# Performance work log

Measured on AMD Instinct MI355X. Metric: run time of the kernel, lower is better.

The kernel has to match this reference:

```python
import jax, jax.numpy as jnp
import numpy as np

B, T = 32, 2048
HID, ACT, SRC, AGE = 512, 64, 2, 16
TRUNK, BINS, PHASES = 256, 20, 7
IN_DIM = HID + ACT + SRC + AGE  # 594


def setup_inputs() -> dict:
    key = jax.random.key(0)
    ks = jax.random.split(key, 16)
    s_in = 1.0 / np.sqrt(IN_DIM)
    s_tr = 1.0 / np.sqrt(TRUNK)
    s_h = 1.0 / np.sqrt(HID)
    return {
        "h_t": jax.random.normal(ks[0], (B, T, HID), jnp.float32),
        "a_t": jax.random.normal(ks[1], (B, T, ACT), jnp.float32),
        "d_t": jax.random.normal(ks[2], (B, T, SRC), jnp.float32),
        "age_embed": jax.random.normal(ks[3], (B, T, AGE), jnp.float32),
        "trunk_w": jax.random.normal(ks[4], (IN_DIM, TRUNK), jnp.float32) * s_in,
        "trunk_b": jax.random.normal(ks[5], (TRUNK,), jnp.float32) * s_in,
        "inst_base_w": jax.random.normal(ks[6], (TRUNK, BINS), jnp.float32) * s_tr,
        "inst_base_b": jax.random.normal(ks[7], (BINS,), jnp.float32) * s_tr,
        "group_base_w": jax.random.normal(ks[8], (TRUNK, BINS), jnp.float32) * s_tr,
        "group_base_b": jax.random.normal(ks[9], (BINS,), jnp.float32) * s_tr,
        "inst_exp_w": jax.random.normal(ks[10], (PHASES, TRUNK, BINS), jnp.float32) * s_tr,
        "inst_exp_b": jax.random.normal(ks[11], (PHASES, BINS), jnp.float32) * s_tr,
        "group_exp_w": jax.random.normal(ks[12], (PHASES, TRUNK, BINS), jnp.float32) * s_tr,
        "group_exp_b": jax.random.normal(ks[13], (PHASES, BINS), jnp.float32) * s_tr,
        "router_w": jax.random.normal(ks[14], (HID, PHASES), jnp.float32) * s_h,
        "router_b": jax.random.normal(ks[15], (PHASES,), jnp.float32) * s_h,
    }


def reference(h_t, a_t, d_t, age_embed,
              trunk_w, trunk_b, inst_base_w, inst_base_b,
              group_base_w, group_base_b, inst_exp_w, inst_exp_b,
              group_exp_w, group_exp_b, router_w, router_b):
    # Shared trunk: Linear(594,256) -> exact GELU
    x = jnp.concatenate([h_t, a_t, d_t, age_embed], axis=-1)  # [B,T,594]
    z = jax.nn.gelu(jnp.einsum('bti,io->bto', x, trunk_w) + trunk_b,
                    approximate=False)  # [B,T,256]

    # Soft phase routing from h_t
    pw = jax.nn.softmax(jnp.einsum('bth,hp->btp', h_t, router_w) + router_b,
                        axis=-1)  # [B,T,7]

    # Base heads
    inst_base = jnp.einsum('btd,dk->btk', z, inst_base_w) + inst_base_b
    group_base = jnp.einsum('btd,dk->btk', z, group_base_w) + group_base_b

    # All 7 experts as one batched GEMM, then weighted reduction over phases
    inst_e = jnp.einsum('btd,pdk->btpk', z, inst_exp_w) + inst_exp_b  # [B,T,7,20]
    group_e = jnp.einsum('btd,pdk->btpk', z, group_exp_w) + group_exp_b
    inst_res = jnp.einsum('btp,btpk->btk', pw, inst_e)
    group_res = jnp.einsum('btp,btpk->btk', pw, group_e)

    return (inst_base + inst_res, group_base + group_res)
```

## Files before the change

kernel.cpp:

```cpp
#include <hip/hip_runtime.h>
#include <math.h>

typedef unsigned int uint;
typedef unsigned short ushort;

using short8 = __attribute__((ext_vector_type(8))) short;
using f32x4  = __attribute__((ext_vector_type(4))) float;

#define BT      65536
#define HID     512
#define IN_DIM  594
#define TRUNK   256
#define BINS    20
#define NKCH    19
#define NCOMBO  320

#define WT_P_SZ (19*16*64*8)
#define RP_SZ   (16*64*8)
#define WA_P_SZ (8*20*64*8)

__device__ inline ushort f2bf(float f) {
    uint u = __float_as_uint(f);
    return (ushort)((u + 0x7fffu + ((u >> 16) & 1u)) >> 16);
}

__global__ __launch_bounds__(64) void pack_all(
    const float* __restrict__ trunk_w, const float* __restrict__ router_w,
    const float* __restrict__ inst_base_w, const float* __restrict__ inst_base_b,
    const float* __restrict__ group_base_w, const float* __restrict__ group_base_b,
    const float* __restrict__ inst_exp_w, const float* __restrict__ inst_exp_b,
    const float* __restrict__ group_exp_w, const float* __restrict__ group_exp_b,
    ushort* __restrict__ WtP, ushort* __restrict__ RP,
    ushort* __restrict__ WaP, float* __restrict__ wbias)
{
    const int b = blockIdx.x, l = threadIdx.x;
    const int lr = l & 15, lg = l >> 4;
    if (b < 304) {
        int kk = b >> 4, n = b & 15;
        int col = n * 16 + lr;
        ushort* dst = WtP + ((size_t)(kk * 16 + n) * 64 + l) * 8;
        #pragma unroll
        for (int j = 0; j < 8; ++j) {
            int k = kk * 32 + lg * 8 + j;
            dst[j] = (k < IN_DIM) ? f2bf(trunk_w[k * TRUNK + col]) : (ushort)0;
        }
    } else if (b < 320) {
        int kk = b - 304;
        ushort* dst = RP + ((size_t)(kk * 64 + l)) * 8;
        #pragma unroll
        for (int j = 0; j < 8; ++j) {
            int k = kk * 32 + lg * 8 + j;
            dst[j] = (lr < 7) ? f2bf(router_w[k * 7 + lr]) : (ushort)0;
        }
    } else if (b < 480) {
        int b2 = b - 320, kk = b2 / 20, n = b2 % 20;
        int combo = n * 16 + lr;
        int h = combo / 160, rem = combo % 160, kb = rem >> 3, p = rem & 7;
        const float* bw = h ? group_base_w : inst_base_w;
        const float* ew = h ? group_exp_w  : inst_exp_w;
        ushort* dst = WaP + ((size_t)(kk * 20 + n) * 64 + l) * 8;
        #pragma unroll
        for (int j = 0; j < 8; ++j) {
            int k = kk * 32 + lg * 8 + j;
            float v = (p == 0) ? bw[k * BINS + kb]
                               : ew[((p - 1) * TRUNK + k) * BINS + kb];
            dst[j] = f2bf(v);
        }
    } else {
        for (int c = l; c < NCOMBO; c += 64) {
            int h = c / 160, rem = c % 160, kb = rem >> 3, p = rem & 7;
            const float* bb = h ? group_base_b : inst_base_b;
            const float* eb = h ? group_exp_b  : inst_exp_b;
            wbias[c] = (p == 0) ? bb[kb] : eb[(p - 1) * BINS + kb];
        }
    }
}

__global__ __launch_bounds__(256, 2) void fused_mfma(
    const float* __restrict__ h_t, const float* __restrict__ a_t,
    const float* __restrict__ d_t, const float* __restrict__ age,
    const float* __restrict__ trunk_b, const float* __restrict__ router_b,
    const ushort* __restrict__ WtP, const ushort* __restrict__ RP,
    const ushort* __restrict__ WaP, const float* __restrict__ wbias,
    float* __restrict__ out)
{
    __shared__ alignas(16) ushort smem[32768];

    const int tid = threadIdx.x;
    const int l = tid & 63, w = tid >> 6;
    const int lr = l & 15, lg = l >> 4;
    const int block0 = blockIdx.x * 128;

    const int srow = tid >> 1;
    const int scb  = (tid & 1) * 16;
    const int stok = block0 + srow;

    f32x4 acc[2][16];
    f32x4 accr[2];
    #pragma unroll
    for (int m = 0; m < 2; ++m) {
        accr[m] = (f32x4){0.f, 0.f, 0.f, 0.f};
        #pragma unroll
        for (int n = 0; n < 16; ++n) acc[m][n] = (f32x4){0.f, 0.f, 0.f, 0.f};
    }

    auto stage_load = [&](int kk, float4 ld[4]) {
        int c0 = kk * 32 + scb;
        if (kk < 16) {
            const float4* p = (const float4*)(h_t + (size_t)stok * HID + c0);
            ld[0] = p[0]; ld[1] = p[1]; ld[2] = p[2]; ld[3] = p[3];
        } else if (kk < 18) {
            const float4* p = (const float4*)(a_t + (size_t)stok * 64 + (c0 - 512));
            ld[0] = p[0]; ld[1] = p[1]; ld[2] = p[2]; ld[3] = p[3];
        } else {
            float* f = (float*)ld;
            #pragma unroll
            for (int j = 0; j < 16; ++j) {
                int c = c0 + j;
                float v;
                if (c < 578)        v = d_t[(size_t)stok * 2 + (c - 576)];
                else if (c < 594)   v = age[(size_t)stok * 16 + (c - 578)];
                else                v = 0.f;
                f[j] = v;
            }
        }
    };
    auto stage_write = [&](int buf, float4 ld[4]) {
        const float* f = (const float*)ld;
        short8 v0, v1;
        #pragma unroll
        for (int j = 0; j < 8; ++j) {
            v0[j] = (short)f2bf(f[j]);
            v1[j] = (short)f2bf(f[j + 8]);
        }
        ushort* dst = smem + buf * 4096 + srow * 32 + scb;
        *(short8*)dst = v0;
        *(short8*)(dst + 8) = v1;
    };

    {
        float4 ld[4];
        stage_load(0, ld);
        stage_write(0, ld);
        __syncthreads();
        int cur = 0;
        for (int kk = 0; kk < NKCH; ++kk) {
            float4 nld[4];
            if (kk < NKCH - 1) stage_load(kk + 1, nld);

            const ushort* xa = smem + cur * 4096;
            short8 a0 = *(const short8*)(xa + (w * 32 + lr) * 32 + lg * 8);
            short8 a1 = *(const short8*)(xa + (w * 32 + 16 + lr) * 32 + lg * 8);

            if (kk < 16) {
                short8 rb = *(const short8*)(RP + ((size_t)(kk * 64 + l)) * 8);
                accr[0] = __builtin_amdgcn_mfma_f32_16x16x32_bf16(a0, rb, accr[0], 0, 0, 0);
                accr[1] = __builtin_amdgcn_mfma_f32_16x16x32_bf16(a1, rb, accr[1], 0, 0, 0);
            }
            const ushort* wp = WtP + (size_t)kk * 16 * 64 * 8;
            #pragma unroll
            for (int n = 0; n < 16; ++n) {
                short8 bq = *(const short8*)(wp + ((size_t)n * 64 + l) * 8);
                acc[0][n] = __builtin_amdgcn_mfma_f32_16x16x32_bf16(a0, bq, acc[0][n], 0, 0, 0);
                acc[1][n] = __builtin_amdgcn_mfma_f32_16x16x32_bf16(a1, bq, acc[1][n], 0, 0, 0);
            }
            if (kk < NKCH - 1) stage_write(cur ^ 1, nld);
            __syncthreads();
            cur ^= 1;
        }
    }

    float pwv[2][4];
    {
        const float rb_l = (lr < 7) ? router_b[lr] : 0.f;
        #pragma unroll
        for (int m = 0; m < 2; ++m)
        #pragma unroll
        for (int r = 0; r < 4; ++r) {
            float x = (lr < 7) ? (accr[m][r] + rb_l) : -3.0e38f;
            float mx = x;
            mx = fmaxf(mx, __shfl_xor(mx, 1));
            mx = fmaxf(mx, __shfl_xor(mx, 2));
            mx = fmaxf(mx, __shfl_xor(mx, 4));
            mx = fmaxf(mx, __shfl_xor(mx, 8));
            float e = expf(x - mx);
            float s = e;
            s += __shfl_xor(s, 1);
            s += __shfl_xor(s, 2);
            s += __shfl_xor(s, 4);
            s += __shfl_xor(s, 8);
            pwv[m][r] = e / s;
        }
    }

    {
        float tb_[16];
        #pragma unroll
        for (int n = 0; n < 16; ++n) tb_[n] = trunk_b[n * 16 + lr];
        char* zb = (char*)smem;
        #pragma unroll
        for (int m = 0; m < 2; ++m)
        #pragma unroll
        for (int n = 0; n < 16; ++n)
        #pragma unroll
        for (int r = 0; r < 4; ++r) {
            float v = acc[m][n][r] + tb_[n];
            v = 0.5f * v * (1.f + erff(v * 0.70710678118654752f));
            int row  = w * 32 + m * 16 + lg * 4 + r;
            int col  = n * 16 + lr;
            int slot = (col >> 3) ^ (row & 7);
            *(ushort*)(zb + row * 512 + slot * 16 + (col & 7) * 2) = f2bf(v);
        }
    }
    __syncthreads();

    const char* zb = (const char*)smem;
    const int p8 = l & 7;
    const int csrc = (l & 48) | (p8 ? (p8 - 1) : 0);
    const int row0 = w * 32 + lr;
    const int row1 = row0 + 16;
    #pragma unroll 1
    for (int hf = 0; hf < 2; ++hf) {
        f32x4 acc2[2][10];
        #pragma unroll
        for (int m = 0; m < 2; ++m)
        #pragma unroll
        for (int n = 0; n < 10; ++n) acc2[m][n] = (f32x4){0.f, 0.f, 0.f, 0.f};
        float wb_[10];
        #pragma unroll
        for (int n = 0; n < 10; ++n) wb_[n] = wbias[(hf * 10 + n) * 16 + lr];

        #pragma unroll
        for (int kk = 0; kk < 8; ++kk) {
            short8 a0 = *(const short8*)(zb + row0 * 512 + (((kk * 4 + lg) ^ (row0 & 7)) << 4));
            short8 a1 = *(const short8*)(zb + row1 * 512 + (((kk * 4 + lg) ^ (row1 & 7)) << 4));
            const ushort* wp = WaP + (size_t)(kk * 20 + hf * 10) * 64 * 8;
            #pragma unroll
            for (int n = 0; n < 10; ++n) {
                short8 bq = *(const short8*)(wp + ((size_t)n * 64 + l) * 8);
                acc2[0][n] = __builtin_amdgcn_mfma_f32_16x16x32_bf16(a0, bq, acc2[0][n], 0, 0, 0);
                acc2[1][n] = __builtin_amdgcn_mfma_f32_16x16x32_bf16(a1, bq, acc2[1][n], 0, 0, 0);
            }
        }

        #pragma unroll
        for (int m = 0; m < 2; ++m)
        #pragma unroll
        for (int n = 0; n < 10; ++n)
        #pragma unroll
        for (int r = 0; r < 4; ++r) {
            float e = acc2[m][n][r] + wb_[n];
            float c = __shfl(pwv[m][r], csrc);
            float coef = p8 ? c : 1.0f;
            float val = coef * e;
            val += __shfl_xor(val, 1);
            val += __shfl_xor(val, 2);
            val += __shfl_xor(val, 4);
            if (p8 == 0) {
                int combo = (hf * 10 + n) * 16 + lr;
                int h = combo / 160, rem = combo % 160, kb = rem >> 3;
                int t = block0 + w * 32 + m * 16 + lg * 4 + r;
                out[(size_t)h * (BT * BINS) + (size_t)t * BINS + kb] = val;
            }
        }
    }
}

extern "C" void kernel_launch(void* const* d_in, const int* in_sizes, int n_in,
                              void* d_out, int out_size, void* d_ws, size_t ws_size,
                              hipStream_t stream) {
    const float* h_t          = (const float*)d_in[0];
    const float* a_t          = (const float*)d_in[1];
    const float* d_t          = (const float*)d_in[2];
    const float* age_embed    = (const float*)d_in[3];
    const float* trunk_w      = (const float*)d_in[4];
    const float* trunk_b      = (const float*)d_in[5];
    const float* inst_base_w  = (const float*)d_in[6];
    const float* inst_base_b  = (const float*)d_in[7];
    const float* group_base_w = (const float*)d_in[8];
    const float* group_base_b = (const float*)d_in[9];
    const float* inst_exp_w   = (const float*)d_in[10];
    const float* inst_exp_b   = (const float*)d_in[11];
    const float* group_exp_w  = (const float*)d_in[12];
    const float* group_exp_b  = (const float*)d_in[13];
    const float* router_w     = (const float*)d_in[14];
    const float* router_b     = (const float*)d_in[15];

    ushort* WtP  = (ushort*)d_ws;
    ushort* RP   = WtP + WT_P_SZ;
    ushort* WaP  = RP + RP_SZ;
    float*  wbias = (float*)(WaP + WA_P_SZ);

    pack_all<<<481, 64, 0, stream>>>(
        trunk_w, router_w,
        inst_base_w, inst_base_b, group_base_w, group_base_b,
        inst_exp_w, inst_exp_b, group_exp_w, group_exp_b,
        WtP, RP, WaP, wbias);

    fused_mfma<<<BT / 128, 256, 0, stream>>>(
        h_t, a_t, d_t, age_embed, trunk_b, router_b,
        WtP, RP, WaP, wbias, (float*)d_out);
}
```

Measured before the change: 108.3 us.

## Load activations directly into MFMA registers and drop LDS staging and barriers

The trunk GEMM no longer stages activation tiles through double-buffered shared memory. Each lane now loads its own rows straight from global memory into the MFMA A-operand registers, which removes the per-chunk __syncthreads and LDS round trips. The z write and the second GEMM drop the barrier between them, since each wave reads back only its own rows. The head GEMM is merged from two 10-column halves into one 20-column pass, which raises register pressure (40 accumulators) and risks spills or lower occupancy under launch_bounds(256,2), and loses the software prefetch of global loads.

```diff
diff --git a/kernel.cpp b/kernel.cpp
--- a/kernel.cpp
+++ b/kernel.cpp
@@ -84,16 +84,14 @@
     const ushort* __restrict__ WaP, const float* __restrict__ wbias,
     float* __restrict__ out)
 {
-    __shared__ alignas(16) ushort smem[32768];
+    __shared__ alignas(16) ushort zs[128 * 256];
 
     const int tid = threadIdx.x;
     const int l = tid & 63, w = tid >> 6;
     const int lr = l & 15, lg = l >> 4;
     const int block0 = blockIdx.x * 128;
-
-    const int srow = tid >> 1;
-    const int scb  = (tid & 1) * 16;
-    const int stok = block0 + srow;
+    const size_t tok0 = block0 + w * 32 + lr;
+    const size_t tok1 = tok0 + 16;
 
     f32x4 acc[2][16];
     f32x4 accr[2];
@@ -104,69 +102,70 @@
         for (int n = 0; n < 16; ++n) acc[m][n] = (f32x4){0.f, 0.f, 0.f, 0.f};
     }
 
-    auto stage_load = [&](int kk, float4 ld[4]) {
-        int c0 = kk * 32 + scb;
-        if (kk < 16) {
-            const float4* p = (const float4*)(h_t + (size_t)stok * HID + c0);
-            ld[0] = p[0]; ld[1] = p[1]; ld[2] = p[2]; ld[3] = p[3];
-        } else if (kk < 18) {
-            const float4* p = (const float4*)(a_t + (size_t)stok * 64 + (c0 - 512));
-            ld[0] = p[0]; ld[1] = p[1]; ld[2] = p[2]; ld[3] = p[3];
-        } else {
-            float* f = (float*)ld;
-            #pragma unroll
-            for (int j = 0; j < 16; ++j) {
-                int c = c0 + j;
-                float v;
-                if (c < 578)        v = d_t[(size_t)stok * 2 + (c - 576)];
-                else if (c < 594)   v = age[(size_t)stok * 16 + (c - 578)];
-                else                v = 0.f;
-                f[j] = v;
-            }
-        }
+    auto cvt8 = [](float4 a, float4 b) -> short8 {
+        short8 v;
+        v[0] = (short)f2bf(a.x); v[1] = (short)f2bf(a.y);
+        v[2] = (short)f2bf(a.z); v[3] = (short)f2bf(a.w);
+        v[4] = (short)f2bf(b.x); v[5] = (short)f2bf(b.y);
+        v[6] = (short)f2bf(b.z); v[7] = (short)f2bf(b.w);
+        return v;
     };
-    auto stage_write = [&](int buf, float4 ld[4]) {
-        const float* f = (const float*)ld;
-        short8 v0, v1;
+
+    #pragma unroll 2
+    for (int kk = 0; kk < 16; ++kk) {
+        const float4* p0 = (const float4*)(h_t + tok0 * HID + kk * 32 + lg * 8);
+        const float4* p1 = (const float4*)(h_t + tok1 * HID + kk * 32 + lg * 8);
+        float4 f00 = p0[0], f01 = p0[1];
+        float4 f10 = p1[0], f11 = p1[1];
+        short8 a0 = cvt8(f00, f01);
+        short8 a1 = cvt8(f10, f11);
+
+        short8 rb = *(const short8*)(RP + ((size_t)(kk * 64 + l)) * 8);
+        accr[0] = __builtin_amdgcn_mfma_f32_16x16x32_bf16(a0, rb, accr[0], 0, 0, 0);
+        accr[1] = __builtin_amdgcn_mfma_f32_16x16x32_bf16(a1, rb, accr[1], 0, 0, 0);
+
+        const ushort* wp = WtP + (size_t)kk * 16 * 64 * 8;
+        #pragma unroll
+        for (int n = 0; n < 16; ++n) {
+            short8 bq = *(const short8*)(wp + ((size_t)n * 64 + l) * 8);
+            acc[0][n] = __builtin_amdgcn_mfma_f32_16x16x32_bf16(a0, bq, acc[0][n], 0, 0, 0);
+            acc[1][n] = __builtin_amdgcn_mfma_f32_16x16x32_bf16(a1, bq, acc[1][n], 0, 0, 0);
+        }
+    }
+    #pragma unroll
+    for (int kk = 16; kk < 18; ++kk) {
+        const float4* p0 = (const float4*)(a_t + tok0 * 64 + (kk - 16) * 32 + lg * 8);
+        const float4* p1 = (const float4*)(a_t + tok1 * 64 + (kk - 16) * 32 + lg * 8);
+        float4 f00 = p0[0], f01 = p0[1];
+        float4 f10 = p1[0], f11 = p1[1];
+        short8 a0 = cvt8(f00, f01);
+        short8 a1 = cvt8(f10, f11);
+        const ushort* wp = WtP + (size_t)kk * 16 * 64 * 8;
+        #pragma unroll
+        for (int n = 0; n < 16; ++n) {
+            short8 bq = *(const short8*)(wp + ((size_t)n * 64 + l) * 8);
+            acc[0][n] = __builtin_amdgcn_mfma_f32_16x16x32_bf16(a0, bq, acc[0][n], 0, 0, 0);
+            acc[1][n] = __builtin_amdgcn_mfma_f32_16x16x32_bf16(a1, bq, acc[1][n], 0, 0, 0);
+        }
+    }
+    {
+        short8 a0, a1;
         #pragma unroll
         for (int j = 0; j < 8; ++j) {
-            v0[j] = (short)f2bf(f[j]);
-            v1[j] = (short)f2bf(f[j + 8]);
-        }
-        ushort* dst = smem + buf * 4096 + srow * 32 + scb;
-        *(short8*)dst = v0;
-        *(short8*)(dst + 8) = v1;
-    };
-
-    {
-        float4 ld[4];
-        stage_load(0, ld);
-        stage_write(0, ld);
-        __syncthreads();
-        int cur = 0;
-        for (int kk = 0; kk < NKCH; ++kk) {
-            float4 nld[4];
-            if (kk < NKCH - 1) stage_load(kk + 1, nld);
-
-            const ushort* xa = smem + cur * 4096;
-            short8 a0 = *(const short8*)(xa + (w * 32 + lr) * 32 + lg * 8);
-            short8 a1 = *(const short8*)(xa + (w * 32 + 16 + lr) * 32 + lg * 8);
-
-            if (kk < 16) {
-                short8 rb = *(const short8*)(RP + ((size_t)(kk * 64 + l)) * 8);
-                accr[0] = __builtin_amdgcn_mfma_f32_16x16x32_bf16(a0, rb, accr[0], 0, 0, 0);
-                accr[1] = __builtin_amdgcn_mfma_f32_16x16x32_bf16(a1, rb, accr[1], 0, 0, 0);
-            }
-            const ushort* wp = WtP + (size_t)kk * 16 * 64 * 8;
-            #pragma unroll
-            for (int n = 0; n < 16; ++n) {
-                short8 bq = *(const short8*)(wp + ((size_t)n * 64 + l) * 8);
-                acc[0][n] = __builtin_amdgcn_mfma_f32_16x16x32_bf16(a0, bq, acc[0][n], 0, 0, 0);
-                acc[1][n] = __builtin_amdgcn_mfma_f32_16x16x32_bf16(a1, bq, acc[1][n], 0, 0, 0);
-            }
-            if (kk < NKCH - 1) stage_write(cur ^ 1, nld);
-            __syncthreads();
-            cur ^= 1;
+            int c = 576 + lg * 8 + j;
+            float v0, v1;
+            if (c < 578)      { v0 = d_t[tok0 * 2 + (c - 576)];  v1 = d_t[tok1 * 2 + (c - 576)]; }
+            else if (c < 594) { v0 = age[tok0 * 16 + (c - 578)]; v1 = age[tok1 * 16 + (c - 578)]; }
+            else              { v0 = 0.f; v1 = 0.f; }
+            a0[j] = (short)f2bf(v0);
+            a1[j] = (short)f2bf(v1);
+        }
+        const ushort* wp = WtP + (size_t)18 * 16 * 64 * 8;
+        #pragma unroll
+        for (int n = 0; n < 16; ++n) {
+            short8 bq = *(const short8*)(wp + ((size_t)n * 64 + l) * 8);
+            acc[0][n] = __builtin_amdgcn_mfma_f32_16x16x32_bf16(a0, bq, acc[0][n], 0, 0, 0);
+            acc[1][n] = __builtin_amdgcn_mfma_f32_16x16x32_bf16(a1, bq, acc[1][n], 0, 0, 0);
         }
     }
 
@@ -194,73 +193,75 @@
     }
 
     {
-        float tb_[16];
-        #pragma unroll
-        for (int n = 0; n < 16; ++n) tb_[n] = trunk_b[n * 16 + lr];
-        char* zb = (char*)smem;
-        #pragma unroll
-        for (int m = 0; m < 2; ++m)
-        #pragma unroll
-        for (int n = 0; n < 16; ++n)
-        #pragma unroll
-        for (int r = 0; r < 4; ++r) {
-            float v = acc[m][n][r] + tb_[n];
-            v = 0.5f * v * (1.f + erff(v * 0.70710678118654752f));
-            int row  = w * 32 + m * 16 + lg * 4 + r;
-            int col  = n * 16 + lr;
-            int slot = (col >> 3) ^ (row & 7);
-            *(ushort*)(zb + row * 512 + slot * 16 + (col & 7) * 2) = f2bf(v);
-        }
-    }
-    __syncthreads();
-
-    const char* zb = (const char*)smem;
+        char* zb = (char*)zs;
+        #pragma unroll
+        for (int n = 0; n < 16; ++n) {
+            float tb = trunk_b[n * 16 + lr];
+            #pragma unroll
+            for (int m = 0; m < 2; ++m)
+            #pragma unroll
+            for (int r = 0; r < 4; ++r) {
+                float v = acc[m][n][r] + tb;
+                v = 0.5f * v * (1.f + erff(v * 0.70710678118654752f));
+                int row  = w * 32 + m * 16 + lg * 4 + r;
+                int col  = n * 16 + lr;
+                int slot = (col >> 3) ^ (row & 7);
+                *(ushort*)(zb + row * 512 + slot * 16 + (col & 7) * 2) = f2bf(v);
+            }
+        }
+    }
+
+    const char* zb = (const char*)zs;
     const int p8 = l & 7;
     const int csrc = (l & 48) | (p8 ? (p8 - 1) : 0);
     const int row0 = w * 32 + lr;
     const int row1 = row0 + 16;
-    #pragma unroll 1
-    for (int hf = 0; hf < 2; ++hf) {
-        f32x4 acc2[2][10];
+
+    f32x4 acc2[2][20];
+    #pragma unroll
+    for (int m = 0; m < 2; ++m)
+    #pragma unroll
+    for (int n = 0; n < 20; ++n) acc2[m][n] = (f32x4){0.f, 0.f, 0.f, 0.f};
+
+    #pragma unroll
+    for (int kk = 0; kk < 8; ++kk) {
+        short8 a0 = *(const short8*)(zb + row0 * 512 + (((kk * 4 + lg) ^ (row0 & 7)) << 4));
+        short8 a1 = *(const short8*)(zb + row1 * 512 + (((kk * 4 + lg) ^ (row1 & 7)) << 4));
+        const ushort* wp = WaP + (size_t)(kk * 20) * 64 * 8;
+        #pragma unroll
+        for (int n = 0; n < 20; ++n) {
+            short8 bq = *(const short8*)(wp + ((size_t)n * 64 + l) * 8);
+            acc2[0][n] = __builtin_amdgcn_mfma_f32_16x16x32_bf16(a0, bq, acc2[0][n], 0, 0, 0);
+            acc2[1][n] = __builtin_amdgcn_mfma_f32_16x16x32_bf16(a1, bq, acc2[1][n], 0, 0, 0);
+        }
+    }
+
+    {
+        float cw[2][4];
         #pragma unroll
         for (int m = 0; m < 2; ++m)
         #pragma unroll
-        for (int n = 0; n < 10; ++n) acc2[m][n] = (f32x4){0.f, 0.f, 0.f, 0.f};
-        float wb_[10];
-        #pragma unroll
-        for (int n = 0; n < 10; ++n) wb_[n] = wbias[(hf * 10 + n) * 16 + lr];
-
-        #pragma unroll
-        for (int kk = 0; kk < 8; ++kk) {
-            short8 a0 = *(const short8*)(zb + row0 * 512 + (((kk * 4 + lg) ^ (row0 & 7)) << 4));
-            short8 a1 = *(const short8*)(zb + row1 * 512 + (((kk * 4 + lg) ^ (row1 & 7)) << 4));
-            const ushort* wp = WaP + (size_t)(kk * 20 + hf * 10) * 64 * 8;
+        for (int r = 0; r < 4; ++r)
+            cw[m][r] = __shfl(pwv[m][r], csrc);
+
+        #pragma unroll
+        for (int n = 0; n < 20; ++n) {
+            float wb = wbias[n * 16 + lr];
             #pragma unroll
-            for (int n = 0; n < 10; ++n) {
-                short8 bq = *(const short8*)(wp + ((size_t)n * 64 + l) * 8);
-                acc2[0][n] = __builtin_amdgcn_mfma_f32_16x16x32_bf16(a0, bq, acc2[0][n], 0, 0, 0);
-                acc2[1][n] = __builtin_amdgcn_mfma_f32_16x16x32_bf16(a1, bq, acc2[1][n], 0, 0, 0);
-            }
-        }
-
-        #pragma unroll
-        for (int m = 0; m < 2; ++m)
-        #pragma unroll
-        for (int n = 0; n < 10; ++n)
-        #pragma unroll
-        for (int r = 0; r < 4; ++r) {
-            float e = acc2[m][n][r] + wb_[n];
-            float c = __shfl(pwv[m][r], csrc);
-            float coef = p8 ? c : 1.0f;
-            float val = coef * e;
-            val += __shfl_xor(val, 1);
-            val += __shfl_xor(val, 2);
-            val += __shfl_xor(val, 4);
-            if (p8 == 0) {
-                int combo = (hf * 10 + n) * 16 + lr;
-                int h = combo / 160, rem = combo % 160, kb = rem >> 3;
-                int t = block0 + w * 32 + m * 16 + lg * 4 + r;
-                out[(size_t)h * (BT * BINS) + (size_t)t * BINS + kb] = val;
+            for (int m = 0; m < 2; ++m)
+            #pragma unroll
+            for (int r = 0; r < 4; ++r) {
+                float e = acc2[m][n][r] + wb;
+                float val = (p8 ? cw[m][r] : 1.0f) * e;
+                val += __shfl_xor(val, 1);
+                val += __shfl_xor(val, 2);
+                val += __shfl_xor(val, 4);
+                if (p8 == 0) {
+                    int combo = n * 16 + lr;
+                    int h = combo / 160, rem = combo % 160, kb = rem >> 3;
+                    size_t t = block0 + w * 32 + m * 16 + lg * 4 + r;
+                    out[(size_t)h * (BT * BINS) + t * BINS + kb] = val;
+                }
             }
         }
     }
@@ -286,9 +287,9 @@
     const float* router_w     = (const float*)d_in[14];
     const float* router_b     = (const float*)d_in[15];
 
-    ushort* WtP  = (ushort*)d_ws;
-    ushort* RP   = WtP + WT_P_SZ;
-    ushort* WaP  = RP + RP_SZ;
+    ushort* WtP   = (ushort*)d_ws;
+    ushort* RP    = WtP + WT_P_SZ;
+    ushort* WaP   = RP + RP_SZ;
     float*  wbias = (float*)(WaP + WA_P_SZ);
 
     pack_all<<<481, 64, 0, stream>>>(
```

New measurement: 183.2 us. 69.1% more time.

## Split trunk GEMM by output columns per wave instead of rows

Applied to the files above, without the earlier changes.

Each wave now computes all 128 rows for a quarter of the 256 trunk columns (8x4 MFMA tiles) instead of 32 rows over all columns. The activation tile is stored in shared memory in MFMA-fragment order so each wave reads it with one contiguous load per 16-row tile. This cuts the global weight fragments each wave loads per K step from 16 to 4, in exchange for reading 8 activation fragments from shared memory. The router softmax coefficient shuffles are also hoisted out of the head loop.

```diff
diff --git a/kernel.cpp b/kernel.cpp
--- a/kernel.cpp
+++ b/kernel.cpp
@@ -12,7 +12,6 @@
 #define IN_DIM  594
 #define TRUNK   256
 #define BINS    20
-#define NKCH    19
 #define NCOMBO  320
 
 #define WT_P_SZ (19*16*64*8)
@@ -84,7 +83,7 @@
     const ushort* __restrict__ WaP, const float* __restrict__ wbias,
     float* __restrict__ out)
 {
-    __shared__ alignas(16) ushort smem[32768];
+    __shared__ alignas(16) ushort zs[32768];
 
     const int tid = threadIdx.x;
     const int l = tid & 63, w = tid >> 6;
@@ -92,35 +91,35 @@
     const int block0 = blockIdx.x * 128;
 
     const int srow = tid >> 1;
-    const int scb  = (tid & 1) * 16;
-    const int stok = block0 + srow;
-
-    f32x4 acc[2][16];
-    f32x4 accr[2];
+    const int half = tid & 1;
+    const size_t stok = block0 + srow;
+
+    ushort* xs = zs;
+
+    f32x4 acc[8][4];
+    f32x4 accr0 = (f32x4){0.f,0.f,0.f,0.f};
+    f32x4 accr1 = (f32x4){0.f,0.f,0.f,0.f};
     #pragma unroll
-    for (int m = 0; m < 2; ++m) {
-        accr[m] = (f32x4){0.f, 0.f, 0.f, 0.f};
-        #pragma unroll
-        for (int n = 0; n < 16; ++n) acc[m][n] = (f32x4){0.f, 0.f, 0.f, 0.f};
-    }
+    for (int mm = 0; mm < 8; ++mm)
+    #pragma unroll
+    for (int nn = 0; nn < 4; ++nn) acc[mm][nn] = (f32x4){0.f,0.f,0.f,0.f};
 
     auto stage_load = [&](int kk, float4 ld[4]) {
-        int c0 = kk * 32 + scb;
         if (kk < 16) {
-            const float4* p = (const float4*)(h_t + (size_t)stok * HID + c0);
-            ld[0] = p[0]; ld[1] = p[1]; ld[2] = p[2]; ld[3] = p[3];
+            const float4* p = (const float4*)(h_t + stok * HID + kk * 32 + half * 16);
+            ld[0]=p[0]; ld[1]=p[1]; ld[2]=p[2]; ld[3]=p[3];
         } else if (kk < 18) {
-            const float4* p = (const float4*)(a_t + (size_t)stok * 64 + (c0 - 512));
-            ld[0] = p[0]; ld[1] = p[1]; ld[2] = p[2]; ld[3] = p[3];
+            const float4* p = (const float4*)(a_t + stok * 64 + (kk - 16) * 32 + half * 16);
+            ld[0]=p[0]; ld[1]=p[1]; ld[2]=p[2]; ld[3]=p[3];
         } else {
             float* f = (float*)ld;
             #pragma unroll
             for (int j = 0; j < 16; ++j) {
-                int c = c0 + j;
+                int c = 576 + half * 16 + j;
                 float v;
-                if (c < 578)        v = d_t[(size_t)stok * 2 + (c - 576)];
-                else if (c < 594)   v = age[(size_t)stok * 16 + (c - 578)];
-                else                v = 0.f;
+                if (c < 578)      v = d_t[stok * 2 + (c - 576)];
+                else if (c < 594) v = age[stok * 16 + (c - 578)];
+                else              v = 0.f;
                 f[j] = v;
             }
         }
@@ -133,9 +132,9 @@
             v0[j] = (short)f2bf(f[j]);
             v1[j] = (short)f2bf(f[j + 8]);
         }
-        ushort* dst = smem + buf * 4096 + srow * 32 + scb;
+        ushort* dst = xs + buf * 4096 + (srow >> 4) * 512 + ((srow & 15) + half * 32) * 8;
         *(short8*)dst = v0;
-        *(short8*)(dst + 8) = v1;
+        *(short8*)(dst + 128) = v1;
     };
 
     {
@@ -144,27 +143,53 @@
         stage_write(0, ld);
         __syncthreads();
         int cur = 0;
-        for (int kk = 0; kk < NKCH; ++kk) {
+        const int w4 = w * 4;
+        #pragma unroll 1
+        for (int kk = 0; kk < 19; ++kk) {
             float4 nld[4];
-            if (kk < NKCH - 1) stage_load(kk + 1, nld);
-
-            const ushort* xa = smem + cur * 4096;
-            short8 a0 = *(const short8*)(xa + (w * 32 + lr) * 32 + lg * 8);
-            short8 a1 = *(const short8*)(xa + (w * 32 + 16 + lr) * 32 + lg * 8);
+            if (kk < 18) stage_load(kk + 1, nld);
+
+            const ushort* wp = WtP + ((size_t)kk * 16 + w4) * 512;
+            short8 bq0 = *(const short8*)(wp + 0 * 512 + l * 8);
+            short8 bq1 = *(const short8*)(wp + 1 * 512 + l * 8);
+            short8 bq2 = *(const short8*)(wp + 2 * 512 + l * 8);
+            short8 bq3 = *(const short8*)(wp + 3 * 512 + l * 8);
+
+            const ushort* xb = xs + cur * 4096;
+            short8 a0 = *(const short8*)(xb + 0 * 512 + l * 8);
+            short8 a1 = *(const short8*)(xb + 1 * 512 + l * 8);
+            short8 a2 = *(const short8*)(xb + 2 * 512 + l * 8);
+            short8 a3 = *(const short8*)(xb + 3 * 512 + l * 8);
+            short8 a4 = *(const short8*)(xb + 4 * 512 + l * 8);
+            short8 a5 = *(const short8*)(xb + 5 * 512 + l * 8);
+            short8 a6 = *(const short8*)(xb + 6 * 512 + l * 8);
+            short8 a7 = *(const short8*)(xb + 7 * 512 + l * 8);
 
             if (kk < 16) {
-                short8 rb = *(const short8*)(RP + ((size_t)(kk * 64 + l)) * 8);
-                accr[0] = __builtin_amdgcn_mfma_f32_16x16x32_bf16(a0, rb, accr[0], 0, 0, 0);
-                accr[1] = __builtin_amdgcn_mfma_f32_16x16x32_bf16(a1, rb, accr[1], 0, 0, 0);
-            }
-            const ushort* wp = WtP + (size_t)kk * 16 * 64 * 8;
-            #pragma unroll
-            for (int n = 0; n < 16; ++n) {
-                short8 bq = *(const short8*)(wp + ((size_t)n * 64 + l) * 8);
-                acc[0][n] = __builtin_amdgcn_mfma_f32_16x16x32_bf16(a0, bq, acc[0][n], 0, 0, 0);
-                acc[1][n] = __builtin_amdgcn_mfma_f32_16x16x32_bf16(a1, bq, acc[1][n], 0, 0, 0);
-            }
-            if (kk < NKCH - 1) stage_write(cur ^ 1, nld);
+                short8 rb = *(const short8*)(RP + (size_t)kk * 512 + l * 8);
+                short8 ar0 = *(const short8*)(xb + (w * 2 + 0) * 512 + l * 8);
+                short8 ar1 = *(const short8*)(xb + (w * 2 + 1) * 512 + l * 8);
+                accr0 = __builtin_amdgcn_mfma_f32_16x16x32_bf16(ar0, rb, accr0, 0, 0, 0);
+                accr1 = __builtin_amdgcn_mfma_f32_16x16x32_bf16(ar1, rb, accr1, 0, 0, 0);
+            }
+
+            #define TRUNK_MM(AF) \
+                acc[0][0] = __builtin_amdgcn_mfma_f32_16x16x32_bf16(AF, bq0, acc[0][0],0,0,0);
+            #undef TRUNK_MM
+            #pragma unroll
+            for (int nn = 0; nn < 4; ++nn) {
+                short8 bq = (nn == 0) ? bq0 : (nn == 1) ? bq1 : (nn == 2) ? bq2 : bq3;
+                acc[0][nn] = __builtin_amdgcn_mfma_f32_16x16x32_bf16(a0, bq, acc[0][nn],0,0,0);
+                acc[1][nn] = __builtin_amdgcn_mfma_f32_16x16x32_bf16(a1, bq, acc[1][nn],0,0,0);
+                acc[2][nn] = __builtin_amdgcn_mfma_f32_16x16x32_bf16(a2, bq, acc[2][nn],0,0,0);
+                acc[3][nn] = __builtin_amdgcn_mfma_f32_16x16x32_bf16(a3, bq, acc[3][nn],0,0,0);
+                acc[4][nn] = __builtin_amdgcn_mfma_f32_16x16x32_bf16(a4, bq, acc[4][nn],0,0,0);
+                acc[5][nn] = __builtin_amdgcn_mfma_f32_16x16x32_bf16(a5, bq, acc[5][nn],0,0,0);
+                acc[6][nn] = __builtin_amdgcn_mfma_f32_16x16x32_bf16(a6, bq, acc[6][nn],0,0,0);
+                acc[7][nn] = __builtin_amdgcn_mfma_f32_16x16x32_bf16(a7, bq, acc[7][nn],0,0,0);
+            }
+
+            if (kk < 18) stage_write(cur ^ 1, nld);
             __syncthreads();
             cur ^= 1;
         }
@@ -177,7 +202,8 @@
         for (int m = 0; m < 2; ++m)
         #pragma unroll
         for (int r = 0; r < 4; ++r) {
-            float x = (lr < 7) ? (accr[m][r] + rb_l) : -3.0e38f;
+            float lv = (m == 0) ? accr0[r] : accr1[r];
+            float x = (lr < 7) ? (lv + rb_l) : -3.0e38f;
             float mx = x;
             mx = fmaxf(mx, __shfl_xor(mx, 1));
             mx = fmaxf(mx, __shfl_xor(mx, 2));
@@ -194,38 +220,45 @@
     }
 
     {
-        float tb_[16];
-        #pragma unroll
-        for (int n = 0; n < 16; ++n) tb_[n] = trunk_b[n * 16 + lr];
-        char* zb = (char*)smem;
-        #pragma unroll
-        for (int m = 0; m < 2; ++m)
-        #pragma unroll
-        for (int n = 0; n < 16; ++n)
-        #pragma unroll
-        for (int r = 0; r < 4; ++r) {
-            float v = acc[m][n][r] + tb_[n];
-            v = 0.5f * v * (1.f + erff(v * 0.70710678118654752f));
-            int row  = w * 32 + m * 16 + lg * 4 + r;
-            int col  = n * 16 + lr;
-            int slot = (col >> 3) ^ (row & 7);
-            *(ushort*)(zb + row * 512 + slot * 16 + (col & 7) * 2) = f2bf(v);
+        char* zb = (char*)zs;
+        #pragma unroll
+        for (int nn = 0; nn < 4; ++nn) {
+            float tb = trunk_b[(w * 4 + nn) * 16 + lr];
+            int colbase = (w * 4 + nn) * 16 + lr;
+            #pragma unroll
+            for (int mm = 0; mm < 8; ++mm)
+            #pragma unroll
+            for (int r = 0; r < 4; ++r) {
+                float v = acc[mm][nn][r] + tb;
+                v = 0.5f * v * (1.f + erff(v * 0.70710678118654752f));
+                int row  = mm * 16 + lg * 4 + r;
+                int slot = (colbase >> 3) ^ (row & 7);
+                *(ushort*)(zb + row * 512 + slot * 16 + (colbase & 7) * 2) = f2bf(v);
+            }
         }
     }
     __syncthreads();
 
-    const char* zb = (const char*)smem;
+    const char* zb = (const char*)zs;
     const int p8 = l & 7;
     const int csrc = (l & 48) | (p8 ? (p8 - 1) : 0);
     const int row0 = w * 32 + lr;
     const int row1 = row0 + 16;
+
+    float cw[2][4];
+    #pragma unroll
+    for (int m = 0; m < 2; ++m)
+    #pragma unroll
+    for (int r = 0; r < 4; ++r)
+        cw[m][r] = __shfl(pwv[m][r], csrc);
+
     #pragma unroll 1
     for (int hf = 0; hf < 2; ++hf) {
         f32x4 acc2[2][10];
         #pragma unroll
         for (int m = 0; m < 2; ++m)
         #pragma unroll
-        for (int n = 0; n < 10; ++n) acc2[m][n] = (f32x4){0.f, 0.f, 0.f, 0.f};
+        for (int n = 0; n < 10; ++n) acc2[m][n] = (f32x4){0.f,0.f,0.f,0.f};
         float wb_[10];
         #pragma unroll
         for (int n = 0; n < 10; ++n) wb_[n] = wbias[(hf * 10 + n) * 16 + lr];
@@ -234,12 +267,12 @@
         for (int kk = 0; kk < 8; ++kk) {
             short8 a0 = *(const short8*)(zb + row0 * 512 + (((kk * 4 + lg) ^ (row0 & 7)) << 4));
             short8 a1 = *(const short8*)(zb + row1 * 512 + (((kk * 4 + lg) ^ (row1 & 7)) << 4));
-            const ushort* wp = WaP + (size_t)(kk * 20 + hf * 10) * 64 * 8;
+            const ushort* wp = WaP + (size_t)(kk * 20 + hf * 10) * 512;
             #pragma unroll
             for (int n = 0; n < 10; ++n) {
-                short8 bq = *(const short8*)(wp + ((size_t)n * 64 + l) * 8);
-                acc2[0][n] = __builtin_amdgcn_mfma_f32_16x16x32_bf16(a0, bq, acc2[0][n], 0, 0, 0);
-                acc2[1][n] = __builtin_amdgcn_mfma_f32_16x16x32_bf16(a1, bq, acc2[1][n], 0, 0, 0);
+                short8 bq = *(const short8*)(wp + (size_t)n * 512 + l * 8);
+                acc2[0][n] = __builtin_amdgcn_mfma_f32_16x16x32_bf16(a0, bq, acc2[0][n],0,0,0);
+                acc2[1][n] = __builtin_amdgcn_mfma_f32_16x16x32_bf16(a1, bq, acc2[1][n],0,0,0);
             }
         }
 
@@ -250,17 +283,15 @@
         #pragma unroll
         for (int r = 0; r < 4; ++r) {
             float e = acc2[m][n][r] + wb_[n];
-            float c = __shfl(pwv[m][r], csrc);
-            float coef = p8 ? c : 1.0f;
-            float val = coef * e;
+            float val = (p8 ? cw[m][r] : 1.0f) * e;
             val += __shfl_xor(val, 1);
             val += __shfl_xor(val, 2);
             val += __shfl_xor(val, 4);
             if (p8 == 0) {
                 int combo = (hf * 10 + n) * 16 + lr;
                 int h = combo / 160, rem = combo % 160, kb = rem >> 3;
-                int t = block0 + w * 32 + m * 16 + lg * 4 + r;
-                out[(size_t)h * (BT * BINS) + (size_t)t * BINS + kb] = val;
+                size_t t = block0 + w * 32 + m * 16 + lg * 4 + r;
+                out[(size_t)h * (BT * BINS) + t * BINS + kb] = val;
             }
         }
     }
@@ -286,9 +317,9 @@
     const float* router_w     = (const float*)d_in[14];
     const float* router_b     = (const float*)d_in[15];
 
-    ushort* WtP  = (ushort*)d_ws;
-    ushort* RP   = WtP + WT_P_SZ;
-    ushort* WaP  = RP + RP_SZ;
+    ushort* WtP   = (ushort*)d_ws;
+    ushort* RP    = WtP + WT_P_SZ;
+    ushort* WaP   = RP + RP_SZ;
     float*  wbias = (float*)(WaP + WA_P_SZ);
 
     pack_all<<<481, 64, 0, stream>>>(
```

Result: faster. 92.76 us (-14.4%).
